# Kernel tuning notes

Measured on AMD Instinct MI355X. Metric: run time of the kernel, lower is better.

## Reference

```python
import jax, jax.numpy as jnp
import numpy as np

NUM_VIEWS = 11

def setup_inputs() -> dict:
    key = jax.random.key(0)
    ks = jax.random.split(key, 6)
    BF, T, D_IN, D_OUT, R = 128, 196, 1024, 1024, 4
    B = 16
    x = jax.random.normal(ks[0], (BF, T, D_IN), dtype=jnp.float32)
    view_idx = jax.random.randint(ks[1], (B,), 0, NUM_VIEWS)
    W = jax.random.normal(ks[2], (D_OUT, D_IN), dtype=jnp.float32) * (1.0 / np.sqrt(D_IN))
    b = jax.random.normal(ks[3], (D_OUT,), dtype=jnp.float32) * 0.01
    lora_A = jax.random.normal(ks[4], (NUM_VIEWS, D_IN, R), dtype=jnp.float32) * (1.0 / np.sqrt(D_IN))
    lora_B = jax.random.normal(ks[5], (NUM_VIEWS, R, D_OUT), dtype=jnp.float32) * 0.02
    return {"x": x, "view_idx": view_idx, "W": W, "b": b, "lora_A": lora_A, "lora_B": lora_B}

def reference(x, view_idx, W, b, lora_A, lora_B):
    # base linear: [BF, T, D_in] @ [D_in, D_out]
    out = jnp.einsum('bti,oi->bto', x, W) + b
    BF = x.shape[0]
    B = view_idx.shape[0]
    if BF != B:  # static shapes -> Python branch is jit-safe
        curr = jnp.repeat(view_idx, BF // B)  # expand per-frame view index
    else:
        curr = view_idx
    curr = jnp.clip(curr, 0, NUM_VIEWS - 1)
    A = lora_A[curr]          # [BF, D_in, R] gathered per sample
    Bm = lora_B[curr]         # [BF, R, D_out]
    h = jnp.einsum('bti,bir->btr', x, A)      # low-rank projection
    lora = jnp.einsum('btr,bro->bto', h, Bm)  # back to D_out
    return out + lora
```

## Files before the change

kernel.cpp:

```cpp
#include <hip/hip_runtime.h>
#include <hip/hip_bf16.h>
#include <stdint.h>

#define M_TOT 25088
#define N_TOT 1024
#define K_TOT 1024
#define T_LEN 196
#define NVIEW 11
#define ROWS_PER_VIEW 1568

#define BM 128
#define BN 128
#define BK 64

typedef unsigned short u16;
typedef __bf16 bf16x8 __attribute__((ext_vector_type(8)));
typedef float f32x4 __attribute__((ext_vector_type(4)));
typedef unsigned short u16x4 __attribute__((ext_vector_type(4)));

#define XB_ELEMS ((size_t)M_TOT * K_TOT)
#define WB_ELEMS ((size_t)N_TOT * K_TOT)
#define WB_OFF_B (XB_ELEMS * 2)
#define H_OFF_B  (WB_OFF_B + WB_ELEMS * 2)
#define WS_NEEDED (H_OFF_B + (size_t)M_TOT * 4 * 4)

__device__ __forceinline__ u16 f2bf(float f) {
    union { float f; unsigned int i; } c; c.f = f;
    unsigned int i = c.i;
    return (u16)((i + 0x7FFFu + ((i >> 16) & 1u)) >> 16);
}

__global__ __launch_bounds__(256) void prep_kernel(
    const float* __restrict__ x, const float* __restrict__ W,
    const int* __restrict__ view_idx, const float* __restrict__ lora_A,
    u16* __restrict__ xb, u16* __restrict__ wb, float* __restrict__ h) {
    const int wave = threadIdx.x >> 6;
    const int lane = threadIdx.x & 63;
    const int blk  = blockIdx.x;

    if (blk >= M_TOT / 4) {
        const int row = (blk - M_TOT / 4) * 4 + wave;
        const float* src = W + (size_t)row * K_TOT;
        u16* dst = wb + (size_t)row * K_TOT;
#pragma unroll
        for (int it = 0; it < 4; ++it) {
            const int k = it * 256 + lane * 4;
            float4 v = *(const float4*)(src + k);
            u16x4 o = { f2bf(v.x), f2bf(v.y), f2bf(v.z), f2bf(v.w) };
            *(u16x4*)(dst + k) = o;
        }
        return;
    }

    const int row = blk * 4 + wave;
    int v = view_idx[row / ROWS_PER_VIEW];
    v = v < 0 ? 0 : (v > NVIEW - 1 ? NVIEW - 1 : v);
    const float* A  = lora_A + (size_t)v * (K_TOT * 4);
    const float* xr = x + (size_t)row * K_TOT;
    u16* dst = xb + (size_t)row * K_TOT;

#pragma unroll
    for (int it = 0; it < 4; ++it) {
        const int k = it * 256 + lane * 4;
        float4 xv = *(const float4*)(xr + k);
        u16x4 o = { f2bf(xv.x), f2bf(xv.y), f2bf(xv.z), f2bf(xv.w) };
        *(u16x4*)(dst + k) = o;
    }
    float a0 = 0.f, a1 = 0.f, a2 = 0.f, a3 = 0.f;
#pragma unroll
    for (int it = 0; it < 8; ++it) {
        const int k = it * 128 + lane * 2;
        float2 xv = *(const float2*)(xr + k);
        float4 av0 = *(const float4*)(A + (size_t)k * 4);
        float4 av1 = *(const float4*)(A + (size_t)k * 4 + 4);
        a0 += xv.x * av0.x + xv.y * av1.x;
        a1 += xv.x * av0.y + xv.y * av1.y;
        a2 += xv.x * av0.z + xv.y * av1.z;
        a3 += xv.x * av0.w + xv.y * av1.w;
    }
#pragma unroll
    for (int off = 32; off > 0; off >>= 1) {
        a0 += __shfl_xor(a0, off, 64);
        a1 += __shfl_xor(a1, off, 64);
        a2 += __shfl_xor(a2, off, 64);
        a3 += __shfl_xor(a3, off, 64);
    }
    if (lane == 0)
        *(float4*)(h + (size_t)row * 4) = make_float4(a0, a1, a2, a3);
}

__global__ __launch_bounds__(256) void h_only_kernel(
    const float* __restrict__ x, const int* __restrict__ view_idx,
    const float* __restrict__ lora_A, float* __restrict__ h) {
    const int row  = blockIdx.x * 4 + (threadIdx.x >> 6);
    const int lane = threadIdx.x & 63;
    int v = view_idx[row / ROWS_PER_VIEW];
    v = v < 0 ? 0 : (v > NVIEW - 1 ? NVIEW - 1 : v);
    const float* A  = lora_A + (size_t)v * (K_TOT * 4);
    const float* xr = x + (size_t)row * K_TOT;
    float a0 = 0.f, a1 = 0.f, a2 = 0.f, a3 = 0.f;
#pragma unroll
    for (int it = 0; it < 8; ++it) {
        const int k = it * 128 + lane * 2;
        float2 xv = *(const float2*)(xr + k);
        float4 av0 = *(const float4*)(A + (size_t)k * 4);
        float4 av1 = *(const float4*)(A + (size_t)k * 4 + 4);
        a0 += xv.x * av0.x + xv.y * av1.x;
        a1 += xv.x * av0.y + xv.y * av1.y;
        a2 += xv.x * av0.z + xv.y * av1.z;
        a3 += xv.x * av0.w + xv.y * av1.w;
    }
#pragma unroll
    for (int off = 32; off > 0; off >>= 1) {
        a0 += __shfl_xor(a0, off, 64);
        a1 += __shfl_xor(a1, off, 64);
        a2 += __shfl_xor(a2, off, 64);
        a3 += __shfl_xor(a3, off, 64);
    }
    if (lane == 0)
        *(float4*)(h + (size_t)row * 4) = make_float4(a0, a1, a2, a3);
}

template <bool CONV>
__global__ __launch_bounds__(256) void gemm_lora_kernel(
    const void* __restrict__ xp, const void* __restrict__ Wp,
    const float* __restrict__ bias, const int* __restrict__ view_idx,
    const float* __restrict__ lora_B, const float* __restrict__ h,
    float* __restrict__ out) {
    __shared__ u16 As[BM * BK];
    __shared__ u16 Bs[BN * BK];

    const int tid = threadIdx.x;
    const int id = blockIdx.x;
    int bx, by;
    if (id < 1536) { const int c = id >> 6, w = id & 63; by = c * 8 + (w & 7); bx = w >> 3; }
    else           { const int r = id - 1536; by = 192 + (r & 3); bx = r >> 2; }

    const int lane = tid & 63;
    const int wave = tid >> 6;
    const int wm   = (wave >> 1) * 64;
    const int wn   = (wave & 1) * 64;
    const int l16  = lane & 15;
    const int quad = lane >> 4;
    const int sw   = l16 & 7;

    const size_t a_base = (size_t)(by * BM) * K_TOT;
    const size_t b_base = (size_t)(bx * BN) * K_TOT;

    f32x4 acc[4][4] = {};

    for (int kt = 0; kt < K_TOT / BK; ++kt) {
        const int kofs = kt * BK;
        if constexpr (!CONV) {
            const u16* x = (const u16*)xp;
            const u16* W = (const u16*)Wp;
#pragma unroll
            for (int i = 0; i < 4; ++i) {
                const int e = i * 2048 + tid * 8;
                const int r = e >> 6;
                const int c = (((tid & 7) ^ (r & 7)) << 3);
                __builtin_amdgcn_global_load_lds(
                    (const __attribute__((address_space(1))) void*)(x + a_base + (size_t)r * K_TOT + kofs + c),
                    (__attribute__((address_space(3))) void*)(As + e), 16, 0, 0);
                __builtin_amdgcn_global_load_lds(
                    (const __attribute__((address_space(1))) void*)(W + b_base + (size_t)r * K_TOT + kofs + c),
                    (__attribute__((address_space(3))) void*)(Bs + e), 16, 0, 0);
            }
        } else {
            const float* x = (const float*)xp;
            const float* W = (const float*)Wp;
#pragma unroll
            for (int i = 0; i < 8; ++i) {
                const int e = i * 1024 + tid * 4;
                const int r = e >> 6, o = e & 63;
                const int d = r * 64 + (((o >> 3) ^ (r & 7)) << 3) + (o & 7);
                float4 av = *(const float4*)(x + a_base + (size_t)r * K_TOT + kofs + o);
                float4 bv = *(const float4*)(W + b_base + (size_t)r * K_TOT + kofs + o);
                u16x4 ao = { f2bf(av.x), f2bf(av.y), f2bf(av.z), f2bf(av.w) };
                u16x4 bo = { f2bf(bv.x), f2bf(bv.y), f2bf(bv.z), f2bf(bv.w) };
                *(u16x4*)(As + d) = ao;
                *(u16x4*)(Bs + d) = bo;
            }
        }
        __syncthreads();
#pragma unroll
        for (int kk = 0; kk < 2; ++kk) {
            const int csw = (((kk * 4 + quad) ^ sw) << 3);
            bf16x8 a_frag[4], b_frag[4];
#pragma unroll
            for (int mi = 0; mi < 4; ++mi)
                a_frag[mi] = *(const bf16x8*)(const void*)(As + (wm + mi * 16 + l16) * BK + csw);
#pragma unroll
            for (int ni = 0; ni < 4; ++ni)
                b_frag[ni] = *(const bf16x8*)(const void*)(Bs + (wn + ni * 16 + l16) * BK + csw);
#pragma unroll
            for (int mi = 0; mi < 4; ++mi)
#pragma unroll
                for (int ni = 0; ni < 4; ++ni)
                    acc[mi][ni] = __builtin_amdgcn_mfma_f32_16x16x32_bf16(
                        a_frag[mi], b_frag[ni], acc[mi][ni], 0, 0, 0);
        }
        __syncthreads();
    }

    const int rowBase = by * BM + wm;
    const int colBase = bx * BN + wn;
    float biasv[4];
#pragma unroll
    for (int ni = 0; ni < 4; ++ni) biasv[ni] = bias[colBase + ni * 16 + l16];

    const int ve0 = (by * BM) / ROWS_PER_VIEW;
    const int ve1 = (by * BM + BM - 1) / ROWS_PER_VIEW;
    if (ve0 == ve1) {
        int v = view_idx[ve0];
        v = v < 0 ? 0 : (v > NVIEW - 1 ? NVIEW - 1 : v);
        const float* Bv = lora_B + (size_t)v * (4 * N_TOT);
        float Bvv[4][4];
#pragma unroll
        for (int r = 0; r < 4; ++r)
#pragma unroll
            for (int ni = 0; ni < 4; ++ni)
                Bvv[r][ni] = Bv[r * N_TOT + colBase + ni * 16 + l16];
#pragma unroll
        for (int mi = 0; mi < 4; ++mi) {
#pragma unroll
            for (int reg = 0; reg < 4; ++reg) {
                const int grow = rowBase + mi * 16 + quad * 4 + reg;
                const float4 hv = *(const float4*)(h + (size_t)grow * 4);
                float* orow = out + (size_t)grow * N_TOT;
#pragma unroll
                for (int ni = 0; ni < 4; ++ni) {
                    float lora = hv.x * Bvv[0][ni] + hv.y * Bvv[1][ni]
                               + hv.z * Bvv[2][ni] + hv.w * Bvv[3][ni];
                    orow[colBase + ni * 16 + l16] = acc[mi][ni][reg] + biasv[ni] + lora;
                }
            }
        }
    } else {
#pragma unroll
        for (int mi = 0; mi < 4; ++mi) {
#pragma unroll
            for (int reg = 0; reg < 4; ++reg) {
                const int grow = rowBase + mi * 16 + quad * 4 + reg;
                int v = view_idx[grow / ROWS_PER_VIEW];
                v = v < 0 ? 0 : (v > NVIEW - 1 ? NVIEW - 1 : v);
                const float4 hv = *(const float4*)(h + (size_t)grow * 4);
                const float* Bv = lora_B + (size_t)v * (4 * N_TOT);
                float* orow = out + (size_t)grow * N_TOT;
#pragma unroll
                for (int ni = 0; ni < 4; ++ni) {
                    const int gcol = colBase + ni * 16 + l16;
                    float lora = hv.x * Bv[gcol]
                               + hv.y * Bv[N_TOT + gcol]
                               + hv.z * Bv[2 * N_TOT + gcol]
                               + hv.w * Bv[3 * N_TOT + gcol];
                    orow[gcol] = acc[mi][ni][reg] + biasv[ni] + lora;
                }
            }
        }
    }
}

extern "C" void kernel_launch(void* const* d_in, const int* in_sizes, int n_in,
                              void* d_out, int out_size, void* d_ws, size_t ws_size,
                              hipStream_t stream) {
    const float* x        = (const float*)d_in[0];
    const int*   view_idx = (const int*)d_in[1];
    const float* W        = (const float*)d_in[2];
    const float* b        = (const float*)d_in[3];
    const float* lora_A   = (const float*)d_in[4];
    const float* lora_B   = (const float*)d_in[5];
    float* out = (float*)d_out;

    const dim3 ggrid((M_TOT / BM) * (N_TOT / BN));
    if (ws_size >= WS_NEEDED) {
        u16*   xb = (u16*)d_ws;
        u16*   wb = (u16*)((char*)d_ws + WB_OFF_B);
        float* h  = (float*)((char*)d_ws + H_OFF_B);
        hipLaunchKernelGGL(prep_kernel, dim3(M_TOT / 4 + N_TOT / 4), dim3(256), 0, stream,
                           x, W, view_idx, lora_A, xb, wb, h);
        hipLaunchKernelGGL((gemm_lora_kernel<false>), ggrid, dim3(256), 0, stream,
                           xb, wb, b, view_idx, lora_B, h, out);
    } else {
        float* h = (float*)d_ws;
        hipLaunchKernelGGL(h_only_kernel, dim3(M_TOT / 4), dim3(256), 0, stream,
                           x, view_idx, lora_A, h);
        hipLaunchKernelGGL((gemm_lora_kernel<true>), ggrid, dim3(256), 0, stream,
                           x, W, b, view_idx, lora_B, h, out);
    }
}
```

Baseline: 276.8 us.

## Replace bf16 GEMM with 256x256-tile, 8-wave, double-buffered pipelined kernel

Replaces the 128x128 single-buffered bf16 GEMM with a 256x256 tile kernel using 512 threads. LDS is double-buffered and split into halves, so global-to-LDS loads for the next k-step are issued between MFMA quarters, with manual barriers, waitcnts and setprio. A per-XCD-aware block remap assigns tiles. The aim is higher arithmetic intensity and overlap of memory with compute, at the cost of larger register and LDS use and a tail-heavy grid of 392 blocks.

```diff
diff --git a/kernel.cpp b/kernel.cpp
--- a/kernel.cpp
+++ b/kernel.cpp
@@ -5,13 +5,15 @@
 #define M_TOT 25088
 #define N_TOT 1024
 #define K_TOT 1024
-#define T_LEN 196
 #define NVIEW 11
 #define ROWS_PER_VIEW 1568
 
 #define BM 128
 #define BN 128
 #define BK 64
+
+#define GRID256 ((M_TOT / 256) * (N_TOT / 256))
+#define CPX256  (GRID256 / 8)
 
 typedef unsigned short u16;
 typedef __bf16 bf16x8 __attribute__((ext_vector_type(8)));
@@ -23,6 +25,9 @@
 #define WB_OFF_B (XB_ELEMS * 2)
 #define H_OFF_B  (WB_OFF_B + WB_ELEMS * 2)
 #define WS_NEEDED (H_OFF_B + (size_t)M_TOT * 4 * 4)
+
+#define BAR()   asm volatile("s_barrier" ::: "memory")
+#define LGKM0() asm volatile("s_waitcnt lgkmcnt(0)" ::: "memory")
 
 __device__ __forceinline__ u16 f2bf(float f) {
     union { float f; unsigned int i; } c; c.f = f;
@@ -121,96 +126,135 @@
         *(float4*)(h + (size_t)row * 4) = make_float4(a0, a1, a2, a3);
 }
 
-template <bool CONV>
-__global__ __launch_bounds__(256) void gemm_lora_kernel(
-    const void* __restrict__ xp, const void* __restrict__ Wp,
+__device__ __forceinline__ void stage_half(const u16* __restrict__ gpanel,
+                                           u16* lhalf, int kofs, int tid) {
+#pragma unroll
+    for (int ld = 0; ld < 2; ++ld) {
+        const int r = ld * 64 + (tid >> 3);
+        const int c = ((tid & 7) ^ (r & 7)) << 3;
+        __builtin_amdgcn_global_load_lds(
+            (const __attribute__((address_space(1))) void*)(gpanel + (size_t)r * K_TOT + kofs + c),
+            (__attribute__((address_space(3))) void*)(lhalf + ld * 4096 + tid * 8), 16, 0, 0);
+    }
+}
+
+__device__ __forceinline__ void read_a(bf16x8 (&a)[4][2], const u16* Abuf,
+                                       int mi_base, int l16, int quad, int sw) {
+#pragma unroll
+    for (int mi = 0; mi < 4; ++mi)
+#pragma unroll
+        for (int kk = 0; kk < 2; ++kk)
+            a[mi][kk] = *(const bf16x8*)(const void*)(
+                Abuf + ((mi_base + mi) * 16 + l16) * 64 + (((kk * 4 + quad) ^ sw) << 3));
+}
+
+__device__ __forceinline__ void read_b2(bf16x8 (&b)[4][2], const u16* Bbuf, int brow0,
+                                        int ni_base, int l16, int quad, int sw) {
+#pragma unroll
+    for (int ni = 0; ni < 2; ++ni)
+#pragma unroll
+        for (int kk = 0; kk < 2; ++kk)
+            b[ni_base + ni][kk] = *(const bf16x8*)(const void*)(
+                Bbuf + (brow0 + (ni_base + ni) * 16 + l16) * 64 + (((kk * 4 + quad) ^ sw) << 3));
+}
+
+__device__ __forceinline__ void mfma_q(f32x4 (&acc)[8][4], const bf16x8 (&a)[4][2],
+                                       const bf16x8 (&b)[4][2], int mi_off, int ni0) {
+    __builtin_amdgcn_s_setprio(1);
+#pragma unroll
+    for (int mi = 0; mi < 4; ++mi)
+#pragma unroll
+        for (int ni = 0; ni < 2; ++ni)
+#pragma unroll
+            for (int kk = 0; kk < 2; ++kk)
+                acc[mi_off + mi][ni0 + ni] = __builtin_amdgcn_mfma_f32_16x16x32_bf16(
+                    a[mi][kk], b[ni0 + ni][kk], acc[mi_off + mi][ni0 + ni], 0, 0, 0);
+    __builtin_amdgcn_s_setprio(0);
+}
+
+__global__ __launch_bounds__(512, 2) void gemm256_kernel(
+    const u16* __restrict__ xb, const u16* __restrict__ wb,
     const float* __restrict__ bias, const int* __restrict__ view_idx,
     const float* __restrict__ lora_B, const float* __restrict__ h,
     float* __restrict__ out) {
-    __shared__ u16 As[BM * BK];
-    __shared__ u16 Bs[BN * BK];
+    __shared__ u16 As[2][2][8192];
+    __shared__ u16 Bs[2][2][8192];
 
     const int tid = threadIdx.x;
-    const int id = blockIdx.x;
-    int bx, by;
-    if (id < 1536) { const int c = id >> 6, w = id & 63; by = c * 8 + (w & 7); bx = w >> 3; }
-    else           { const int r = id - 1536; by = 192 + (r & 3); bx = r >> 2; }
+    const int id   = blockIdx.x;
+    const int wgid = (id & 7) * CPX256 + (id >> 3);
+    const int by   = wgid >> 2;
+    const int bx   = wgid & 3;
 
     const int lane = tid & 63;
     const int wave = tid >> 6;
-    const int wm   = (wave >> 1) * 64;
-    const int wn   = (wave & 1) * 64;
+    const int wg   = wave >> 2;
+    const int wn   = wave & 3;
     const int l16  = lane & 15;
     const int quad = lane >> 4;
     const int sw   = l16 & 7;
-
-    const size_t a_base = (size_t)(by * BM) * K_TOT;
-    const size_t b_base = (size_t)(bx * BN) * K_TOT;
-
-    f32x4 acc[4][4] = {};
-
-    for (int kt = 0; kt < K_TOT / BK; ++kt) {
-        const int kofs = kt * BK;
-        if constexpr (!CONV) {
-            const u16* x = (const u16*)xp;
-            const u16* W = (const u16*)Wp;
-#pragma unroll
-            for (int i = 0; i < 4; ++i) {
-                const int e = i * 2048 + tid * 8;
-                const int r = e >> 6;
-                const int c = (((tid & 7) ^ (r & 7)) << 3);
-                __builtin_amdgcn_global_load_lds(
-                    (const __attribute__((address_space(1))) void*)(x + a_base + (size_t)r * K_TOT + kofs + c),
-                    (__attribute__((address_space(3))) void*)(As + e), 16, 0, 0);
-                __builtin_amdgcn_global_load_lds(
-                    (const __attribute__((address_space(1))) void*)(W + b_base + (size_t)r * K_TOT + kofs + c),
-                    (__attribute__((address_space(3))) void*)(Bs + e), 16, 0, 0);
-            }
-        } else {
-            const float* x = (const float*)xp;
-            const float* W = (const float*)Wp;
-#pragma unroll
-            for (int i = 0; i < 8; ++i) {
-                const int e = i * 1024 + tid * 4;
-                const int r = e >> 6, o = e & 63;
-                const int d = r * 64 + (((o >> 3) ^ (r & 7)) << 3) + (o & 7);
-                float4 av = *(const float4*)(x + a_base + (size_t)r * K_TOT + kofs + o);
-                float4 bv = *(const float4*)(W + b_base + (size_t)r * K_TOT + kofs + o);
-                u16x4 ao = { f2bf(av.x), f2bf(av.y), f2bf(av.z), f2bf(av.w) };
-                u16x4 bo = { f2bf(bv.x), f2bf(bv.y), f2bf(bv.z), f2bf(bv.w) };
-                *(u16x4*)(As + d) = ao;
-                *(u16x4*)(Bs + d) = bo;
-            }
-        }
-        __syncthreads();
-#pragma unroll
-        for (int kk = 0; kk < 2; ++kk) {
-            const int csw = (((kk * 4 + quad) ^ sw) << 3);
-            bf16x8 a_frag[4], b_frag[4];
-#pragma unroll
-            for (int mi = 0; mi < 4; ++mi)
-                a_frag[mi] = *(const bf16x8*)(const void*)(As + (wm + mi * 16 + l16) * BK + csw);
-#pragma unroll
-            for (int ni = 0; ni < 4; ++ni)
-                b_frag[ni] = *(const bf16x8*)(const void*)(Bs + (wn + ni * 16 + l16) * BK + csw);
-#pragma unroll
-            for (int mi = 0; mi < 4; ++mi)
-#pragma unroll
-                for (int ni = 0; ni < 4; ++ni)
-                    acc[mi][ni] = __builtin_amdgcn_mfma_f32_16x16x32_bf16(
-                        a_frag[mi], b_frag[ni], acc[mi][ni], 0, 0, 0);
-        }
-        __syncthreads();
-    }
-
-    const int rowBase = by * BM + wm;
-    const int colBase = bx * BN + wn;
+    const int bhalf = wn >> 1;
+    const int brow0 = (wn & 1) * 64;
+
+    const u16* Apan0 = xb + (size_t)(by * 256) * K_TOT;
+    const u16* Apan1 = Apan0 + (size_t)128 * K_TOT;
+    const u16* Bpan0 = wb + (size_t)(bx * 256) * K_TOT;
+    const u16* Bpan1 = Bpan0 + (size_t)128 * K_TOT;
+
+    f32x4 acc[8][4] = {};
+
+    stage_half(Apan0, &As[0][0][0], 0, tid);
+    stage_half(Apan1, &As[0][1][0], 0, tid);
+    stage_half(Bpan0, &Bs[0][0][0], 0, tid);
+    stage_half(Bpan1, &Bs[0][1][0], 0, tid);
+    stage_half(Bpan0, &Bs[1][0][0], 64, tid);
+    stage_half(Bpan1, &Bs[1][1][0], 64, tid);
+    asm volatile("s_waitcnt vmcnt(4)" ::: "memory");
+    BAR();
+
+    bf16x8 a[4][2], b[4][2];
+
+    for (int kt = 0; kt < K_TOT / 64; ++kt) {
+        const int buf  = kt & 1;
+        const int nbuf = buf ^ 1;
+        const u16* Abuf = &As[buf][wg][0];
+        const u16* Bbuf = &Bs[buf][bhalf][0];
+
+        if (kt + 1 < 16) stage_half(Apan0, &As[nbuf][0][0], (kt + 1) * 64, tid);
+        read_a(a, Abuf, 0, l16, quad, sw);
+        read_b2(b, Bbuf, brow0, 0, l16, quad, sw);
+        BAR(); LGKM0();
+        mfma_q(acc, a, b, 0, 0);
+        BAR();
+
+        if (kt + 1 < 16) stage_half(Apan1, &As[nbuf][1][0], (kt + 1) * 64, tid);
+        read_b2(b, Bbuf, brow0, 2, l16, quad, sw);
+        BAR(); LGKM0();
+        mfma_q(acc, a, b, 0, 2);
+        BAR();
+
+        if (kt + 2 < 16) stage_half(Bpan0, &Bs[buf][0][0], (kt + 2) * 64, tid);
+        read_a(a, Abuf, 4, l16, quad, sw);
+        BAR(); LGKM0();
+        mfma_q(acc, a, b, 4, 2);
+        BAR();
+
+        if (kt + 2 < 16) stage_half(Bpan1, &Bs[buf][1][0], (kt + 2) * 64, tid);
+        BAR();
+        mfma_q(acc, a, b, 4, 0);
+        if (kt < 14) { asm volatile("s_waitcnt vmcnt(4)" ::: "memory"); }
+        else         { asm volatile("s_waitcnt vmcnt(0)" ::: "memory"); }
+        BAR();
+    }
+
+    const int rowBase = by * 256 + wg * 128;
+    const int colBase = bx * 256 + wn * 64;
     float biasv[4];
 #pragma unroll
     for (int ni = 0; ni < 4; ++ni) biasv[ni] = bias[colBase + ni * 16 + l16];
 
-    const int ve0 = (by * BM) / ROWS_PER_VIEW;
-    const int ve1 = (by * BM + BM - 1) / ROWS_PER_VIEW;
+    const int ve0 = (by * 256) / ROWS_PER_VIEW;
+    const int ve1 = (by * 256 + 255) / ROWS_PER_VIEW;
     if (ve0 == ve1) {
         int v = view_idx[ve0];
         v = v < 0 ? 0 : (v > NVIEW - 1 ? NVIEW - 1 : v);
@@ -222,7 +266,7 @@
             for (int ni = 0; ni < 4; ++ni)
                 Bvv[r][ni] = Bv[r * N_TOT + colBase + ni * 16 + l16];
 #pragma unroll
-        for (int mi = 0; mi < 4; ++mi) {
+        for (int mi = 0; mi < 8; ++mi) {
 #pragma unroll
             for (int reg = 0; reg < 4; ++reg) {
                 const int grow = rowBase + mi * 16 + quad * 4 + reg;
@@ -238,7 +282,7 @@
         }
     } else {
 #pragma unroll
-        for (int mi = 0; mi < 4; ++mi) {
+        for (int mi = 0; mi < 8; ++mi) {
 #pragma unroll
             for (int reg = 0; reg < 4; ++reg) {
                 const int grow = rowBase + mi * 16 + quad * 4 + reg;
@@ -256,6 +300,96 @@
                                + hv.w * Bv[3 * N_TOT + gcol];
                     orow[gcol] = acc[mi][ni][reg] + biasv[ni] + lora;
                 }
+            }
+        }
+    }
+}
+
+__global__ __launch_bounds__(256) void gemm_conv_kernel(
+    const float* __restrict__ xp, const float* __restrict__ Wp,
+    const float* __restrict__ bias, const int* __restrict__ view_idx,
+    const float* __restrict__ lora_B, const float* __restrict__ h,
+    float* __restrict__ out) {
+    __shared__ u16 As[BM * BK];
+    __shared__ u16 Bs[BN * BK];
+
+    const int tid = threadIdx.x;
+    const int id = blockIdx.x;
+    int bx, by;
+    if (id < 1536) { const int c = id >> 6, w = id & 63; by = c * 8 + (w & 7); bx = w >> 3; }
+    else           { const int r = id - 1536; by = 192 + (r & 3); bx = r >> 2; }
+
+    const int lane = tid & 63;
+    const int wave = tid >> 6;
+    const int wm   = (wave >> 1) * 64;
+    const int wn   = (wave & 1) * 64;
+    const int l16  = lane & 15;
+    const int quad = lane >> 4;
+    const int sw   = l16 & 7;
+
+    const size_t a_base = (size_t)(by * BM) * K_TOT;
+    const size_t b_base = (size_t)(bx * BN) * K_TOT;
+
+    f32x4 acc[4][4] = {};
+
+    for (int kt = 0; kt < K_TOT / BK; ++kt) {
+        const int kofs = kt * BK;
+#pragma unroll
+        for (int i = 0; i < 8; ++i) {
+            const int e = i * 1024 + tid * 4;
+            const int r = e >> 6, o = e & 63;
+            const int d = r * 64 + (((o >> 3) ^ (r & 7)) << 3) + (o & 7);
+            float4 av = *(const float4*)(xp + a_base + (size_t)r * K_TOT + kofs + o);
+            float4 bv = *(const float4*)(Wp + b_base + (size_t)r * K_TOT + kofs + o);
+            u16x4 ao = { f2bf(av.x), f2bf(av.y), f2bf(av.z), f2bf(av.w) };
+            u16x4 bo = { f2bf(bv.x), f2bf(bv.y), f2bf(bv.z), f2bf(bv.w) };
+            *(u16x4*)(As + d) = ao;
+            *(u16x4*)(Bs + d) = bo;
+        }
+        __syncthreads();
+#pragma unroll
+        for (int kk = 0; kk < 2; ++kk) {
+            const int csw = (((kk * 4 + quad) ^ sw) << 3);
+            bf16x8 a_frag[4], b_frag[4];
+#pragma unroll
+            for (int mi = 0; mi < 4; ++mi)
+                a_frag[mi] = *(const bf16x8*)(const void*)(As + (wm + mi * 16 + l16) * BK + csw);
+#pragma unroll
+            for (int ni = 0; ni < 4; ++ni)
+                b_frag[ni] = *(const bf16x8*)(const void*)(Bs + (wn + ni * 16 + l16) * BK + csw);
+#pragma unroll
+            for (int mi = 0; mi < 4; ++mi)
+#pragma unroll
+                for (int ni = 0; ni < 4; ++ni)
+                    acc[mi][ni] = __builtin_amdgcn_mfma_f32_16x16x32_bf16(
+                        a_frag[mi], b_frag[ni], acc[mi][ni], 0, 0, 0);
+        }
+        __syncthreads();
+    }
+
+    const int rowBase = by * BM + wm;
+    const int colBase = bx * BN + wn;
+    float biasv[4];
+#pragma unroll
+    for (int ni = 0; ni < 4; ++ni) biasv[ni] = bias[colBase + ni * 16 + l16];
+#pragma unroll
+    for (int mi = 0; mi < 4; ++mi) {
+#pragma unroll
+        for (int reg = 0; reg < 4; ++reg) {
+            const int grow = rowBase + mi * 16 + quad * 4 + reg;
+            int v = view_idx[grow / ROWS_PER_VIEW];
+            v = v < 0 ? 0 : (v > NVIEW - 1 ? NVIEW - 1 : v);
+            const float4 hv = *(const float4*)(h + (size_t)grow * 4);
+            const float* Bv = lora_B + (size_t)v * (4 * N_TOT);
+            float* orow = out + (size_t)grow * N_TOT;
+#pragma unroll
+            for (int ni = 0; ni < 4; ++ni) {
+                const int gcol = colBase + ni * 16 + l16;
+                float lora = hv.x * Bv[gcol]
+                           + hv.y * Bv[N_TOT + gcol]
+                           + hv.z * Bv[2 * N_TOT + gcol]
+                           + hv.w * Bv[3 * N_TOT + gcol];
+                orow[gcol] = acc[mi][ni][reg] + biasv[ni] + lora;
             }
         }
     }
@@ -272,20 +406,19 @@
     const float* lora_B   = (const float*)d_in[5];
     float* out = (float*)d_out;
 
-    const dim3 ggrid((M_TOT / BM) * (N_TOT / BN));
     if (ws_size >= WS_NEEDED) {
         u16*   xb = (u16*)d_ws;
         u16*   wb = (u16*)((char*)d_ws + WB_OFF_B);
         float* h  = (float*)((char*)d_ws + H_OFF_B);
         hipLaunchKernelGGL(prep_kernel, dim3(M_TOT / 4 + N_TOT / 4), dim3(256), 0, stream,
                            x, W, view_idx, lora_A, xb, wb, h);
-        hipLaunchKernelGGL((gemm_lora_kernel<false>), ggrid, dim3(256), 0, stream,
+        hipLaunchKernelGGL(gemm256_kernel, dim3(GRID256), dim3(512), 0, stream,
                            xb, wb, b, view_idx, lora_B, h, out);
     } else {
         float* h = (float*)d_ws;
         hipLaunchKernelGGL(h_only_kernel, dim3(M_TOT / 4), dim3(256), 0, stream,
                            x, view_idx, lora_A, h);
-        hipLaunchKernelGGL((gemm_lora_kernel<true>), ggrid, dim3(256), 0, stream,
+        hipLaunchKernelGGL(gemm_conv_kernel, dim3((M_TOT / BM) * (N_TOT / BN)), dim3(256), 0, stream,
                            x, W, b, view_idx, lora_B, h, out);
     }
 }
```

Result: slower. 283.0 us (+2.2%).
